# Optimization experiments

Hardware: AMD Instinct MI355X
Metric: run time of the kernel (lower is better)

The kernel has to match this reference:

```python
import jax, jax.numpy as jnp
import numpy as np

F_DIM = 64      # self.n_atom_basis inside blocks (= n_atom_basis // 2)
N_LAYERS = 2
N_RBF = 20
CUTOFF = 5.0
EPS = 1e-8
N_ATOMS = 15000
N_PAIRS = 300000


def setup_inputs() -> dict:
    key = jax.random.key(0)
    ks = jax.random.split(key, 20)
    def w(k, shape, fan_in):
        return (jax.random.normal(k, shape, dtype=jnp.float32) / np.float32(np.sqrt(fan_in)))
    F, L, R = F_DIM, N_LAYERS, N_RBF
    return {
        "Z": jax.random.randint(ks[0], (N_ATOMS,), 0, 100),
        "Rij": jax.random.normal(ks[1], (N_PAIRS, 3), dtype=jnp.float32),
        "idx_i": jax.random.randint(ks[2], (N_PAIRS,), 0, N_ATOMS),
        "idx_j": jax.random.randint(ks[3], (N_PAIRS,), 0, N_ATOMS),
        "n_atoms": N_ATOMS,
        "embed": w(ks[4], (100, F), 1.0),
        "filter_W": w(ks[5], (R, L * 3 * F), R),
        "filter_b": jnp.zeros((L * 3 * F,), jnp.float32),
        "ctx_W1": w(ks[6], (L, F, F), F),
        "ctx_b1": jnp.zeros((L, F), jnp.float32),
        "ctx_W2": w(ks[7], (L, F, 3 * F), F),
        "ctx_b2": jnp.zeros((L, 3 * F), jnp.float32),
        "comp_W1": w(ks[8], (L, 2 * F, 32), 2 * F),
        "comp_b1": jnp.zeros((L, 32), jnp.float32),
        "comp_W2": w(ks[9], (L, 32, F), 32),
        "comp_b2": jnp.zeros((L, F), jnp.float32),
        "rec_W1": w(ks[10], (L, F, 32), F),
        "rec_b1": jnp.zeros((L, 32), jnp.float32),
        "rec_W2": w(ks[11], (L, 32, F * F), 32),
        "rec_b2": jnp.zeros((L, F * F), jnp.float32),
        "mix_W1": w(ks[12], (L, 2 * F, F), 2 * F),
        "mix_b1": jnp.zeros((L, F), jnp.float32),
        "mix_W2": w(ks[13], (L, F, 3 * F), F),
        "mix_b2": jnp.zeros((L, 3 * F), jnp.float32),
        "mu_mix_W": w(ks[14], (L, F, 2 * F), F),
    }


def _compress(v, W1, b1, W2, b2):
    # v: [..., 3, C]  (xyz axis = -2). Per-channel vector norm -> MLP -> softmax weights.
    s = jnp.sqrt(jnp.sum(v * v, axis=-2) + EPS)                      # [..., C]
    wts = jax.nn.softmax(jnp.maximum(s @ W1 + b1, 0.0) @ W2 + b2, axis=-1)  # [..., Fc]
    # einsum('bvc,bl->blc') == weights (outer) sum_over_channels(v)
    return jnp.sum(v, axis=-1, keepdims=True) * wts[..., None, :]    # [..., 3, Fc]


def _interaction(q, mu, Wij, dir_ij, idx_i, idx_j, n_atoms,
                 cW1, cb1, cW2, cb2, pW1, pb1, pW2, pb2, rW1, rb1, rW2, rb2):
    F = q.shape[-1]
    x = jax.nn.silu(q @ cW1 + cb1) @ cW2 + cb2                       # [n,1,3F]
    xe = x[idx_j] * Wij                                               # [p,1,3F] gather + filter mult
    dq, dmuR, dmumu = jnp.split(xe, 3, axis=-1)
    dq = jax.ops.segment_sum(dq, idx_i, num_segments=n_atoms)        # [n,1,F]
    cvj = _compress(mu[idx_j], pW1, pb1, pW2, pb2)                    # [p,3,F]
    dmu = dmuR * dir_ij[:, :, None] + dmumu * cvj                     # [p,3,F]
    dmu = jax.ops.segment_sum(dmu, idx_i, num_segments=n_atoms)       # [n,3,F]
    cvi = _compress(mu, pW1, pb1, pW2, pb2)                           # [n,3,F]
    q = q + dq
    mu = dmu + cvi                                                    # [n,3,F]
    # reconstruction layer -> rank-2 tensors per channel
    cv = jnp.swapaxes(mu, 1, 2)                                       # [n,F,3]
    s = jnp.sqrt(jnp.sum(mu * mu, axis=1) + EPS)                      # [n,F]
    sw = (jnp.maximum(s @ rW1 + rb1, 0.0) @ rW2 + rb2).reshape(-1, F, F)
    dtm = jnp.einsum('nrc,nci,ncj->nrij', sw, cv, cv)                 # [n,F,3,3]
    return q, mu, dtm


def _mixing(q, mu, dtm, W1, b1, W2, b2, Wm):
    mu_mix = mu @ Wm                                                  # [n,3,2F]
    mu_V, mu_W = jnp.split(mu_mix, 2, axis=-1)
    mu_Vn = jnp.sqrt(jnp.sum(mu_V * mu_V, axis=-2, keepdims=True) + EPS)  # [n,1,F]
    x = jax.nn.silu(jnp.concatenate([q, mu_Vn], axis=-1) @ W1 + b1) @ W2 + b2
    dq_i, dmu_i, dqmu_i = jnp.split(x, 3, axis=-1)
    dmu_i = dmu_i * mu_W
    dqmu_i = dqmu_i * jnp.sum(mu_V * mu_W, axis=1, keepdims=True)
    q = q + dq_i + dqmu_i                                             # [n,1,F]
    tv = jnp.einsum('nfij,njf->nif', dtm, mu)                         # [n,3,F]
    mu = jnp.concatenate([mu + dmu_i, tv], axis=-1)                   # [n,3,2F]
    return q, mu


def _forward(Z, Rij, idx_i, idx_j, n_atoms, embed, filter_W, filter_b,
             ctx_W1, ctx_b1, ctx_W2, ctx_b2, comp_W1, comp_b1, comp_W2, comp_b2,
             rec_W1, rec_b1, rec_W2, rec_b2, mix_W1, mix_b1, mix_W2, mix_b2, mu_mix_W):
    F = embed.shape[1]
    d = jnp.linalg.norm(Rij, axis=1, keepdims=True)                   # [p,1]
    dir_ij = Rij / d                                                  # [p,3]
    offsets = jnp.linspace(0.0, CUTOFF, N_RBF).astype(jnp.float32)
    width = offsets[1] - offsets[0]
    phi = jnp.exp(-0.5 * ((d[..., None] - offsets) / width) ** 2)     # [p,1,R]
    fcut = 0.5 * (jnp.cos(jnp.pi * d / CUTOFF) + 1.0) * (d < CUTOFF)  # [p,1]
    filters = (phi @ filter_W + filter_b) * fcut[..., None]           # [p,1,L*3F]
    q = embed[Z][:, None, :]                                          # [n,1,F]
    mu = jnp.zeros((q.shape[0], 3, 2 * F), q.dtype)                   # [n,3,2F]
    for l in range(ctx_W1.shape[0]):
        Wij = filters[..., l * 3 * F:(l + 1) * 3 * F]
        q, mu, dtm = _interaction(q, mu, Wij, dir_ij, idx_i, idx_j, n_atoms,
                                  ctx_W1[l], ctx_b1[l], ctx_W2[l], ctx_b2[l],
                                  comp_W1[l], comp_b1[l], comp_W2[l], comp_b2[l],
                                  rec_W1[l], rec_b1[l], rec_W2[l], rec_b2[l])
        q, mu = _mixing(q, mu, dtm, mix_W1[l], mix_b1[l], mix_W2[l], mix_b2[l], mu_mix_W[l])
    return q[:, 0, :], mu  # scalar_representation [n,F], vector_representation [n,3,2F]


def reference(Z, Rij, idx_i, idx_j, n_atoms, embed, filter_W, filter_b,
              ctx_W1, ctx_b1, ctx_W2, ctx_b2, comp_W1, comp_b1, comp_W2, comp_b2,
              rec_W1, rec_b1, rec_W2, rec_b2, mix_W1, mix_b1, mix_W2, mix_b2, mu_mix_W):
    return _forward(Z, Rij, idx_i, idx_j, n_atoms, embed, filter_W, filter_b,
                    ctx_W1, ctx_b1, ctx_W2, ctx_b2, comp_W1, comp_b1, comp_W2, comp_b2,
                    rec_W1, rec_b1, rec_W2, rec_b2, mix_W1, mix_b1, mix_W2, mix_b2, mu_mix_W)
```

## Files before the change

### kernel.cpp

```cpp
#include <hip/hip_runtime.h>
#include <math.h>

#define FD 64
#define NRBF 20
#define CUT 5.0f
#define EPSV 1e-8f
#define PI_F 3.14159265358979f

typedef _Float16 h2v __attribute__((ext_vector_type(2)));

__device__ __forceinline__ float wredsum(float v){
#pragma unroll
  for (int m = 32; m >= 1; m >>= 1) v += __shfl_xor(v, m, 64);
  return v;
}
__device__ __forceinline__ float wredmax(float v){
#pragma unroll
  for (int m = 32; m >= 1; m >>= 1) v = fmaxf(v, __shfl_xor(v, m, 64));
  return v;
}
__device__ __forceinline__ float silu_f(float x){ return x * (1.0f / (1.0f + __expf(-x))); }
__device__ __forceinline__ h2v as_h2(unsigned u){
  union { unsigned u; h2v h; } x; x.u = u; return x.h;
}
__device__ __forceinline__ unsigned pack_bf16(float a, float b){
  unsigned ua = __float_as_uint(a), ub = __float_as_uint(b);
  ua = (ua + 0x7fffu + ((ua >> 16) & 1u)) >> 16;
  ub = (ub + 0x7fffu + ((ub >> 16) & 1u)) >> 16;
  return ua | (ub << 16);
}
__device__ __forceinline__ unsigned pack_f16(float a, float b){
  return __builtin_bit_cast(unsigned, __builtin_amdgcn_cvt_pkrtz(a, b));
}
#define BF_LO(u) __uint_as_float((u) << 16)
#define BF_HI(u) __uint_as_float((u) & 0xffff0000u)

__global__ __launch_bounds__(256) void k_count(const int* __restrict__ idx_i,
                                               int* __restrict__ cnt, int P)
{
  int p = blockIdx.x * blockDim.x + threadIdx.x;
  if (p < P) atomicAdd(&cnt[idx_i[p]], 1);
}

__global__ __launch_bounds__(1024) void k_scan(const int* __restrict__ cnt,
                                               int* __restrict__ start,
                                               int* __restrict__ cursor, int N)
{
  __shared__ int part[1024];
  int t = threadIdx.x;
  int chunk = (N + 1023) / 1024;
  int lo = t * chunk, hi = lo + chunk; if (hi > N) hi = N;
  int s = 0;
  for (int i = lo; i < hi; ++i) s += cnt[i];
  part[t] = s;
  __syncthreads();
  for (int off = 1; off < 1024; off <<= 1){
    int v = 0;
    if (t >= off) v = part[t - off];
    __syncthreads();
    if (t >= off) part[t] += v;
    __syncthreads();
  }
  int run = (t == 0) ? 0 : part[t-1];
  for (int i = lo; i < hi; ++i){ start[i] = run; cursor[i] = run; run += cnt[i]; }
  if (t == 1023) start[N] = run;
}

__global__ __launch_bounds__(256) void k_scatter(const int* __restrict__ idx_i,
                                                 int* __restrict__ cursor,
                                                 int* __restrict__ elist, int P)
{
  int p = blockIdx.x * blockDim.x + threadIdx.x;
  if (p < P){
    int pos = atomicAdd(&cursor[idx_i[p]], 1);
    elist[pos] = p;
  }
}

__global__ __launch_bounds__(256) void k_edgeprep(const float* __restrict__ Rij,
                                                  const int* __restrict__ elist,
                                                  const int* __restrict__ idx_j,
                                                  float* __restrict__ eP,
                                                  int* __restrict__ eJ, int P)
{
  int e = blockIdx.x * blockDim.x + threadIdx.x;
  if (e >= P) return;
  int p = elist[e];
  eJ[e] = idx_j[p];
  float rx = Rij[3*p+0], ry = Rij[3*p+1], rz = Rij[3*p+2];
  float d = sqrtf(rx*rx + ry*ry + rz*rz);
  float inv = 1.0f / d;
  float fc = (d < CUT) ? 0.5f * (__cosf(PI_F * d / CUT) + 1.0f) : 0.0f;
  float* pr = eP + (size_t)e * 16;
  pr[0] = rx*inv; pr[1] = ry*inv; pr[2] = rz*inv; pr[3] = fc;
  const float width = CUT / (float)(NRBF - 1);
  float ph[NRBF];
#pragma unroll
  for (int r = 0; r < NRBF; ++r){
    float t = (d - width * (float)r) / width;
    ph[r] = __expf(-0.5f * t * t) * fc;
  }
  unsigned* pu = (unsigned*)(pr + 4);
#pragma unroll
  for (int r = 0; r < 10; ++r) pu[r] = pack_f16(ph[2*r], ph[2*r+1]);
  pr[14] = 0.f; pr[15] = 0.f;
}

__global__ __launch_bounds__(256) void k_transpose_w(const float* __restrict__ rW2,
                                                     const float* __restrict__ rb2,
                                                     unsigned short* __restrict__ rW2S,
                                                     float* __restrict__ rb2T)
{
  int t = blockIdx.x * blockDim.x + threadIdx.x;
  if (t < 2*64*64*32){
    int km = t & 7;
    int f  = (t >> 3) & 63;
    int kq = (t >> 9) & 3;
    int c  = (t >> 11) & 63;
    int l  = t >> 17;
    int k  = kq*8 + km;
    float v = rW2[((size_t)(l*32 + k))*4096 + f*64 + c];
    _Float16 hv = (_Float16)v;
    unsigned short us;
    __builtin_memcpy(&us, &hv, 2);
    rW2S[t] = us;
  }
  if (t < 2*64*64){
    int f = t & 63, c = (t >> 6) & 63, l = t >> 12;
    rb2T[t] = rb2[(size_t)l*4096 + f*64 + c];
  }
}

__global__ __launch_bounds__(256) void k_init_q(const int* __restrict__ Z,
                                                const float* __restrict__ embed,
                                                float* __restrict__ q, int Ntot)
{
  int t = blockIdx.x * blockDim.x + threadIdx.x;
  if (t >= Ntot * FD) return;
  int n = t >> 6, f = t & 63;
  q[t] = embed[Z[n]*FD + f];
}

__global__ __launch_bounds__(256) void k_atom_pre(
    const float* __restrict__ q, const float* __restrict__ mu,
    const float* __restrict__ cW1, const float* __restrict__ cb1,
    const float* __restrict__ cW2, const float* __restrict__ cb2,
    const float* __restrict__ pW1, const float* __restrict__ pb1,
    const float* __restrict__ pW2, const float* __restrict__ pb2,
    unsigned* __restrict__ XCVh, float* __restrict__ CVf, int Ntot)
{
  __shared__ float wbuf[12288];
  __shared__ float qs[16][64];
  __shared__ float sbuf[16][128];
  __shared__ float h1s[16][64];
  __shared__ float hcs[16][32];
  int t = threadIdx.x;
  int w = t >> 6, f = t & 63;
  int base = blockIdx.x * 16;
  const int aw = w * 4;
  float4* wt4 = (float4*)wbuf;

  float m0a[4], m1a[4], m2a[4], m0b[4], m1b[4], m2b[4];
#pragma unroll
  for (int s = 0; s < 4; ++s){
    int a = aw + s;
    int n = base + a; if (n >= Ntot) n = Ntot - 1;
    qs[a][f] = q[(size_t)n*64 + f];
    const float* mun = mu + (size_t)n * 384;
    m0a[s] = mun[0*128 + f];      m1a[s] = mun[1*128 + f];      m2a[s] = mun[2*128 + f];
    m0b[s] = mun[0*128 + 64 + f]; m1b[s] = mun[1*128 + 64 + f]; m2b[s] = mun[2*128 + 64 + f];
    sbuf[a][f]      = sqrtf(m0a[s]*m0a[s] + m1a[s]*m1a[s] + m2a[s]*m2a[s] + EPSV);
    sbuf[a][64 + f] = sqrtf(m0b[s]*m0b[s] + m1b[s]*m1b[s] + m2b[s]*m2b[s] + EPSV);
  }
#pragma unroll
  for (int i = 0; i < 4; ++i) wt4[t + i*256] = ((const float4*)cW1)[t + i*256];
  __syncthreads();

  float hacc[4];
#pragma unroll
  for (int s = 0; s < 4; ++s) hacc[s] = cb1[f];
  for (int k = 0; k < 64; ++k){
    float wv = wbuf[k*64 + f];
#pragma unroll
    for (int s = 0; s < 4; ++s) hacc[s] = fmaf(qs[aw + s][k], wv, hacc[s]);
  }
#pragma unroll
  for (int s = 0; s < 4; ++s) h1s[aw + s][f] = silu_f(hacc[s]);

  __syncthreads();
#pragma unroll
  for (int i = 0; i < 12; ++i) wt4[t + i*256] = ((const float4*)cW2)[t + i*256];
  __syncthreads();

  float x0[4], x1[4], x2[4];
#pragma unroll
  for (int s = 0; s < 4; ++s){ x0[s] = cb2[f]; x1[s] = cb2[64+f]; x2[s] = cb2[128+f]; }
  for (int k = 0; k < 64; ++k){
    float u0 = wbuf[k*192 + f];
    float u1 = wbuf[k*192 + 64 + f];
    float u2 = wbuf[k*192 + 128 + f];
#pragma unroll
    for (int s = 0; s < 4; ++s){
      float h = h1s[aw + s][k];
      x0[s] = fmaf(h, u0, x0[s]); x1[s] = fmaf(h, u1, x1[s]); x2[s] = fmaf(h, u2, x2[s]);
    }
  }
#pragma unroll
  for (int s = 0; s < 4; ++s){
    int n = base + aw + s;
    if (n < Ntot) XCVh[(size_t)n*192 + f] = pack_bf16(x0[s], x1[s]);
  }

  __syncthreads();
#pragma unroll
  for (int i = 0; i < 4; ++i) wt4[t + i*256] = ((const float4*)pW1)[t + i*256];
#pragma unroll
  for (int i = 0; i < 2; ++i) wt4[1024 + t + i*256] = ((const float4*)pW2)[t + i*256];
  __syncthreads();

  int ki = f & 31;
#pragma unroll
  for (int p = 0; p < 2; ++p){
    int a_h = aw + p*2 + (f >> 5);
    float ah = pb1[ki];
#pragma unroll 4
    for (int c = 0; c < 128; ++c) ah = fmaf(sbuf[a_h][c], wbuf[c*32 + ki], ah);
    hcs[a_h][ki] = fmaxf(ah, 0.0f);
  }

  float logit[4];
#pragma unroll
  for (int s = 0; s < 4; ++s) logit[s] = pb2[f];
  for (int k = 0; k < 32; ++k){
    float wv = wbuf[4096 + k*64 + f];
#pragma unroll
    for (int s = 0; s < 4; ++s) logit[s] = fmaf(hcs[aw + s][k], wv, logit[s]);
  }
#pragma unroll
  for (int s = 0; s < 4; ++s){
    float mx = wredmax(logit[s]);
    float e  = __expf(logit[s] - mx);
    float se = wredsum(e);
    float wt = e / se;
    float v0 = wredsum(m0a[s] + m0b[s]);
    float v1 = wredsum(m1a[s] + m1b[s]);
    float v2 = wredsum(m2a[s] + m2b[s]);
    int n = base + aw + s;
    if (n < Ntot){
      float cv0 = v0 * wt, cv1 = v1 * wt, cv2 = v2 * wt;
      XCVh[(size_t)n*192 + 64 + f]  = pack_bf16(x2[s], cv0);
      XCVh[(size_t)n*192 + 128 + f] = pack_bf16(cv1, cv2);
      float* cvn = CVf + (size_t)n*192;
      cvn[f] = cv0; cvn[64+f] = cv1; cvn[128+f] = cv2;
    }
  }
}

__global__ __launch_bounds__(256) void k_gather(
    const float* __restrict__ eP, const int* __restrict__ eJ,
    const int* __restrict__ start,
    const float* __restrict__ fW, const float* __restrict__ fb,
    const unsigned* __restrict__ XCVh,
    float* __restrict__ dq, float* __restrict__ dmu, int l, int Ntot)
{
  int w = threadIdx.x >> 6;
  int f = threadIdx.x & 63;
  int i = blockIdx.x * 4 + w;
  if (i >= Ntot) return;
  const int col = l * 192;

  unsigned fwp0[10], fwp1[10], fwp2[10];
#pragma unroll
  for (int r = 0; r < 10; ++r){
    const float* fa = fW + (2*r)*384 + col;
    const float* fbp = fW + (2*r+1)*384 + col;
    fwp0[r] = pack_f16(fa[f],       fbp[f]);
    fwp1[r] = pack_f16(fa[64 + f],  fbp[64 + f]);
    fwp2[r] = pack_f16(fa[128 + f], fbp[128 + f]);
  }
  float fb0 = fb[col + f], fb1 = fb[col + 64 + f], fb2 = fb[col + 128 + f];

  float dqa = 0.f, dm0 = 0.f, dm1 = 0.f, dm2 = 0.f;
  int e0 = start[i], e1 = start[i+1];
  int e = e0;
  for (; e + 4 <= e1; e += 4){
    int jj[4];
    float4 d4[4];
    uint4  p0[4], p1[4], p2[4];
    unsigned xv0[4], xv1[4], xv2[4];
#pragma unroll
    for (int u = 0; u < 4; ++u) jj[u] = eJ[e + u];
#pragma unroll
    for (int u = 0; u < 4; ++u){
      const float4* pr = (const float4*)(eP + (size_t)(e + u) * 16);
      const uint4*  pui = (const uint4*)pr;
      d4[u] = pr[0]; p0[u] = pui[1]; p1[u] = pui[2]; p2[u] = pui[3];
    }
#pragma unroll
    for (int u = 0; u < 4; ++u){
      const unsigned* xj = XCVh + (size_t)jj[u] * 192;
      xv0[u] = xj[f]; xv1[u] = xj[64 + f]; xv2[u] = xj[128 + f];
    }
#pragma unroll
    for (int u = 0; u < 4; ++u){
      unsigned ph[10] = {p0[u].x,p0[u].y,p0[u].z,p0[u].w,
                         p1[u].x,p1[u].y,p1[u].z,p1[u].w,
                         p2[u].x,p2[u].y};
      float fc = d4[u].w;
      float w0 = fb0 * fc, w1 = fb1 * fc, w2 = fb2 * fc;
#pragma unroll
      for (int r = 0; r < 10; ++r){
        w0 = __builtin_amdgcn_fdot2(as_h2(ph[r]), as_h2(fwp0[r]), w0, false);
        w1 = __builtin_amdgcn_fdot2(as_h2(ph[r]), as_h2(fwp1[r]), w1, false);
        w2 = __builtin_amdgcn_fdot2(as_h2(ph[r]), as_h2(fwp2[r]), w2, false);
      }
      dqa = fmaf(BF_LO(xv0[u]), w0, dqa);
      float dmR = BF_HI(xv0[u]) * w1, dmm = BF_LO(xv1[u]) * w2;
      dm0 = fmaf(dmR, d4[u].x, fmaf(dmm, BF_HI(xv1[u]), dm0));
      dm1 = fmaf(dmR, d4[u].y, fmaf(dmm, BF_LO(xv2[u]), dm1));
      dm2 = fmaf(dmR, d4[u].z, fmaf(dmm, BF_HI(xv2[u]), dm2));
    }
  }
  for (; e < e1; ++e){
    int j = eJ[e];
    const float4* pr = (const float4*)(eP + (size_t)e * 16);
    const uint4*  pu = (const uint4*)pr;
    float4 A0 = pr[0];
    uint4  Ap0 = pu[1], Ap1 = pu[2], Ap2 = pu[3];
    const unsigned* xj = XCVh + (size_t)j * 192;
    unsigned u0=xj[f], u1=xj[64+f], u2=xj[128+f];
    unsigned ph[10] = {Ap0.x,Ap0.y,Ap0.z,Ap0.w, Ap1.x,Ap1.y,Ap1.z,Ap1.w, Ap2.x,Ap2.y};
    float w0 = fb0 * A0.w, w1 = fb1 * A0.w, w2 = fb2 * A0.w;
#pragma unroll
    for (int r = 0; r < 10; ++r){
      w0 = __builtin_amdgcn_fdot2(as_h2(ph[r]), as_h2(fwp0[r]), w0, false);
      w1 = __builtin_amdgcn_fdot2(as_h2(ph[r]), as_h2(fwp1[r]), w1, false);
      w2 = __builtin_amdgcn_fdot2(as_h2(ph[r]), as_h2(fwp2[r]), w2, false);
    }
    dqa = fmaf(BF_LO(u0), w0, dqa);
    float dmR = BF_HI(u0) * w1, dmm = BF_LO(u1) * w2;
    dm0 = fmaf(dmR, A0.x, fmaf(dmm, BF_HI(u1), dm0));
    dm1 = fmaf(dmR, A0.y, fmaf(dmm, BF_LO(u2), dm1));
    dm2 = fmaf(dmR, A0.z, fmaf(dmm, BF_HI(u2), dm2));
  }
  dq[(size_t)i*64 + f] = dqa;
  float* dmn = dmu + (size_t)i*192;
  dmn[f] = dm0; dmn[64 + f] = dm1; dmn[128 + f] = dm2;
}

__global__ __launch_bounds__(512) void k_tv(
    const float* __restrict__ dmuA, const float* __restrict__ CVf,
    const float* __restrict__ rW1, const float* __restrict__ rb1,
    const unsigned short* __restrict__ rW2S, const float* __restrict__ rb2Tl,
    float* __restrict__ MUI, float* __restrict__ TV, int Ntot)
{
  __shared__ float mus[16][3][64];
  __shared__ float svs[16][64];
  __shared__ float4 wt4[2048];
  __shared__ float rbt[8][64];
  int t = threadIdx.x;
  int w = t >> 6, f = t & 63;
  int base = blockIdx.x * 16;

#pragma unroll
  for (int s = 0; s < 2; ++s){
    int a = w*2 + s;
    int n = base + a; bool ok = (n < Ntot); if (!ok) n = Ntot - 1;
    const float* dmn = dmuA + (size_t)n*192;
    const float* cvn = CVf  + (size_t)n*192;
    float m0 = dmn[f]       + cvn[f];
    float m1 = dmn[64 + f]  + cvn[64 + f];
    float m2 = dmn[128 + f] + cvn[128 + f];
    mus[a][0][f] = m0; mus[a][1][f] = m1; mus[a][2][f] = m2;
    svs[a][f] = sqrtf(m0*m0 + m1*m1 + m2*m2 + EPSV);
    if (ok){
      float* mo = MUI + (size_t)n*192;
      mo[f] = m0; mo[64+f] = m1; mo[128+f] = m2;
    }
  }
  __syncthreads();

  int ki = f & 31;
  int a_h = w*2 + (f >> 5);
  float ah = rb1[ki];
#pragma unroll
  for (int c = 0; c < 64; ++c) ah = fmaf(svs[a_h][c], rW1[c*32 + ki], ah);
  ah = fmaxf(ah, 0.0f);
  unsigned hpk0[16], hpk1[16];
#pragma unroll
  for (int k = 0; k < 16; ++k){
    float a0 = __shfl(ah, 2*k, 64),      b0 = __shfl(ah, 2*k + 1, 64);
    float a1 = __shfl(ah, 32 + 2*k, 64), b1 = __shfl(ah, 32 + 2*k + 1, 64);
    hpk0[k] = pack_f16(a0, b0);
    hpk1[k] = pack_f16(a1, b1);
  }

  const int a0i = w*2, a1i = a0i + 1;
  float mf00 = mus[a0i][0][f], mf01 = mus[a0i][1][f], mf02 = mus[a0i][2][f];
  float mf10 = mus[a1i][0][f], mf11 = mus[a1i][1][f], mf12 = mus[a1i][2][f];
  float tv00=0,tv01=0,tv02=0, tv10=0,tv11=0,tv12=0;
  const uint4* wtu = reinterpret_cast<const uint4*>(wt4);

  for (int ct = 0; ct < 8; ++ct){
    __syncthreads();
    const float4* src = (const float4*)rW2S + (size_t)ct*2048;
#pragma unroll
    for (int i = 0; i < 4; ++i) wt4[t + i*512] = src[t + i*512];
    if (t < 128) ((float4*)rbt)[t] = ((const float4*)(rb2Tl + ct*512))[t];
    __syncthreads();

#pragma unroll
    for (int cc = 0; cc < 8; ++cc){
      int c = ct*8 + cc;
      float u00 = mus[a0i][0][c], u01 = mus[a0i][1][c], u02 = mus[a0i][2][c];
      float u10 = mus[a1i][0][c], u11 = mus[a1i][1][c], u12 = mus[a1i][2][c];
      float g0 = u00*mf00 + u01*mf01 + u02*mf02;
      float g1 = u10*mf10 + u11*mf11 + u12*mf12;
      float acc0 = rbt[cc][f];
      float acc1 = acc0;
#pragma unroll
      for (int kq = 0; kq < 4; ++kq){
        uint4 u = wtu[(cc*4 + kq)*64 + f];
        int k0 = kq*4;
        acc0 = __builtin_amdgcn_fdot2(as_h2(u.x), as_h2(hpk0[k0+0]), acc0, false);
        acc0 = __builtin_amdgcn_fdot2(as_h2(u.y), as_h2(hpk0[k0+1]), acc0, false);
        acc0 = __builtin_amdgcn_fdot2(as_h2(u.z), as_h2(hpk0[k0+2]), acc0, false);
        acc0 = __builtin_amdgcn_fdot2(as_h2(u.w), as_h2(hpk0[k0+3]), acc0, false);
        acc1 = __builtin_amdgcn_fdot2(as_h2(u.x), as_h2(hpk1[k0+0]), acc1, false);
        acc1 = __builtin_amdgcn_fdot2(as_h2(u.y), as_h2(hpk1[k0+1]), acc1, false);
        acc1 = __builtin_amdgcn_fdot2(as_h2(u.z), as_h2(hpk1[k0+2]), acc1, false);
        acc1 = __builtin_amdgcn_fdot2(as_h2(u.w), as_h2(hpk1[k0+3]), acc1, false);
      }
      float mm0 = acc0 * g0, mm1 = acc1 * g1;
      tv00 = fmaf(u00, mm0, tv00); tv01 = fmaf(u01, mm0, tv01); tv02 = fmaf(u02, mm0, tv02);
      tv10 = fmaf(u10, mm1, tv10); tv11 = fmaf(u11, mm1, tv11); tv12 = fmaf(u12, mm1, tv12);
    }
  }

  int n0 = base + a0i, n1 = base + a1i;
  if (n0 < Ntot){
    float* tvp = TV + (size_t)n0*192;
    tvp[f] = tv00; tvp[64+f] = tv01; tvp[128+f] = tv02;
  }
  if (n1 < Ntot){
    float* tvp = TV + (size_t)n1*192;
    tvp[f] = tv10; tvp[64+f] = tv11; tvp[128+f] = tv12;
  }
}

__global__ __launch_bounds__(256) void k_mix2(
    float* __restrict__ q, float* __restrict__ mu,
    const float* __restrict__ dq, const float* __restrict__ MUI, const float* __restrict__ TV,
    const float* __restrict__ mW1, const float* __restrict__ mb1,
    const float* __restrict__ mW2, const float* __restrict__ mb2,
    const float* __restrict__ Wm, int Ntot)
{
  __shared__ float wbuf[12288];
  __shared__ float mua[16][3][64];
  __shared__ float ava[16][128];
  __shared__ float h2a[16][64];
  int t = threadIdx.x;
  int w = t >> 6, f = t & 63;
  int base = blockIdx.x * 16;
  const int aw = w * 4;
  float4* wt4 = (float4*)wbuf;

  float qv[4], m0[4], m1[4], m2[4];
#pragma unroll
  for (int s = 0; s < 4; ++s){
    int a = aw + s;
    int n = base + a; if (n >= Ntot) n = Ntot - 1;
    qv[s] = q[(size_t)n*64 + f] + dq[(size_t)n*64 + f];
    const float* mi = MUI + (size_t)n*192;
    m0[s] = mi[f]; m1[s] = mi[64 + f]; m2[s] = mi[128 + f];
    mua[a][0][f] = m0[s]; mua[a][1][f] = m1[s]; mua[a][2][f] = m2[s];
  }

#pragma unroll
  for (int i = 0; i < 8; ++i) wt4[t + i*256] = ((const float4*)Wm)[t + i*256];
  __syncthreads();

  float V0[4]={0,0,0,0}, V1[4]={0,0,0,0}, V2[4]={0,0,0,0};
  float W0[4]={0,0,0,0}, W1[4]={0,0,0,0}, W2[4]={0,0,0,0};
  for (int k = 0; k < 64; ++k){
    float wv = wbuf[k*128 + f];
    float ww = wbuf[k*128 + 64 + f];
#pragma unroll
    for (int s = 0; s < 4; ++s){
      int a = aw + s;
      float b0 = mua[a][0][k], b1 = mua[a][1][k], b2 = mua[a][2][k];
      V0[s] = fmaf(b0, wv, V0[s]); V1[s] = fmaf(b1, wv, V1[s]); V2[s] = fmaf(b2, wv, V2[s]);
      W0[s] = fmaf(b0, ww, W0[s]); W1[s] = fmaf(b1, ww, W1[s]); W2[s] = fmaf(b2, ww, W2[s]);
    }
  }
  float dot[4];
#pragma unroll
  for (int s = 0; s < 4; ++s){
    int a = aw + s;
    ava[a][f] = qv[s];
    ava[a][64 + f] = sqrtf(V0[s]*V0[s] + V1[s]*V1[s] + V2[s]*V2[s] + EPSV);
    dot[s] = V0[s]*W0[s] + V1[s]*W1[s] + V2[s]*W2[s];
  }

  __syncthreads();
#pragma unroll
  for (int i = 0; i < 8; ++i) wt4[t + i*256] = ((const float4*)mW1)[t + i*256];
  __syncthreads();

  float acc[4];
#pragma unroll
  for (int s = 0; s < 4; ++s) acc[s] = mb1[f];
  for (int k = 0; k < 128; ++k){
    float wv = wbuf[k*64 + f];
#pragma unroll
    for (int s = 0; s < 4; ++s) acc[s] = fmaf(ava[aw + s][k], wv, acc[s]);
  }
#pragma unroll
  for (int s = 0; s < 4; ++s) h2a[aw + s][f] = silu_f(acc[s]);

  __syncthreads();
#pragma unroll
  for (int i = 0; i < 12; ++i) wt4[t + i*256] = ((const float4*)mW2)[t + i*256];
  __syncthreads();

  float y0[4], y1[4], y2[4];
#pragma unroll
  for (int s = 0; s < 4; ++s){ y0[s] = mb2[f]; y1[s] = mb2[64+f]; y2[s] = mb2[128+f]; }
  for (int k = 0; k < 64; ++k){
    float u0 = wbuf[k*192 + f];
    float u1 = wbuf[k*192 + 64 + f];
    float u2 = wbuf[k*192 + 128 + f];
#pragma unroll
    for (int s = 0; s < 4; ++s){
      float h = h2a[aw + s][k];
      y0[s] = fmaf(h, u0, y0[s]); y1[s] = fmaf(h, u1, y1[s]); y2[s] = fmaf(h, u2, y2[s]);
    }
  }

#pragma unroll
  for (int s = 0; s < 4; ++s){
    int n = base + aw + s;
    if (n < Ntot){
      q[(size_t)n*64 + f] = qv[s] + y0[s] + y2[s]*dot[s];
      const float* tvp = TV + (size_t)n*192;
      float* mun = mu + (size_t)n*384;
      mun[0*128 + f] = fmaf(y1[s], W0[s], m0[s]); mun[0*128 + 64 + f] = tvp[f];
      mun[1*128 + f] = fmaf(y1[s], W1[s], m1[s]); mun[1*128 + 64 + f] = tvp[64+f];
      mun[2*128 + f] = fmaf(y1[s], W2[s], m2[s]); mun[2*128 + 64 + f] = tvp[128+f];
    }
  }
}

extern "C" void kernel_launch(void* const* d_in, const int* in_sizes, int n_in,
                              void* d_out, int out_size, void* d_ws, size_t ws_size,
                              hipStream_t stream)
{
  const int*   Z      = (const int*)  d_in[0];
  const float* Rij    = (const float*)d_in[1];
  const int*   idx_i  = (const int*)  d_in[2];
  const int*   idx_j  = (const int*)  d_in[3];
  const float* embed  = (const float*)d_in[5];
  const float* fW     = (const float*)d_in[6];
  const float* fb     = (const float*)d_in[7];
  const float* ctxW1  = (const float*)d_in[8];
  const float* ctxb1  = (const float*)d_in[9];
  const float* ctxW2  = (const float*)d_in[10];
  const float* ctxb2  = (const float*)d_in[11];
  const float* compW1 = (const float*)d_in[12];
  const float* compb1 = (const float*)d_in[13];
  const float* compW2 = (const float*)d_in[14];
  const float* compb2 = (const float*)d_in[15];
  const float* recW1  = (const float*)d_in[16];
  const float* recb1  = (const float*)d_in[17];
  const float* recW2  = (const float*)d_in[18];
  const float* recb2  = (const float*)d_in[19];
  const float* mixW1  = (const float*)d_in[20];
  const float* mixb1  = (const float*)d_in[21];
  const float* mixW2  = (const float*)d_in[22];
  const float* mixb2  = (const float*)d_in[23];
  const float* muMixW = (const float*)d_in[24];

  const int N = in_sizes[0];
  const int P = in_sizes[1] / 3;

  float* ws    = (float*)d_ws;
  float* eP    = ws;
  float* q     = eP    + (size_t)P*16;
  float* mu    = q     + (size_t)N*64;
  float* XCVhf = mu    + (size_t)N*384;
  float* CVf   = XCVhf + (size_t)N*192;
  float* dq    = CVf   + (size_t)N*192;
  float* dmu   = dq    + (size_t)N*64;
  float* rW2Sf = dmu   + (size_t)N*192;
  float* rb2T  = rW2Sf + (size_t)131072;
  float* TV    = rb2T  + (size_t)8192;
  float* MUI   = TV    + (size_t)N*192;
  int*   cnt    = (int*)(MUI + (size_t)N*192);
  int*   startA = cnt    + N;
  int*   cursor = startA + (N + 1);
  int*   elist  = cursor + N;
  int*   eJ     = elist  + P;
  unsigned*       XCVh = (unsigned*)XCVhf;
  unsigned short* rW2S = (unsigned short*)rW2Sf;

  hipMemsetAsync(mu, 0, (size_t)N*384*sizeof(float), stream);
  hipMemsetAsync(cnt, 0, (size_t)N*sizeof(int), stream);
  k_init_q<<<(N*FD + 255)/256, 256, 0, stream>>>(Z, embed, q, N);
  k_transpose_w<<<(2*64*64*32 + 255)/256, 256, 0, stream>>>(recW2, recb2, rW2S, rb2T);

  k_count<<<(P + 255)/256, 256, 0, stream>>>(idx_i, cnt, P);
  k_scan<<<1, 1024, 0, stream>>>(cnt, startA, cursor, N);
  k_scatter<<<(P + 255)/256, 256, 0, stream>>>(idx_i, cursor, elist, P);
  k_edgeprep<<<(P + 255)/256, 256, 0, stream>>>(Rij, elist, idx_j, eP, eJ, P);

  const int ablk4  = (N + 3) / 4;
  const int ablk16 = (N + 15) / 16;
  for (int l = 0; l < 2; ++l){
    k_atom_pre<<<ablk16, 256, 0, stream>>>(q, mu,
        ctxW1 + (size_t)l*64*64,  ctxb1 + (size_t)l*64,
        ctxW2 + (size_t)l*64*192, ctxb2 + (size_t)l*192,
        compW1 + (size_t)l*128*32, compb1 + (size_t)l*32,
        compW2 + (size_t)l*32*64,  compb2 + (size_t)l*64,
        XCVh, CVf, N);
    k_gather<<<ablk4, 256, 0, stream>>>(eP, eJ, startA, fW, fb, XCVh,
        dq, dmu, l, N);
    k_tv<<<ablk16, 512, 0, stream>>>(dmu, CVf,
        recW1 + (size_t)l*64*32, recb1 + (size_t)l*32,
        rW2S + (size_t)l*131072, rb2T + (size_t)l*4096,
        MUI, TV, N);
    k_mix2<<<ablk16, 256, 0, stream>>>(q, mu, dq, MUI, TV,
        mixW1 + (size_t)l*128*64, mixb1 + (size_t)l*64,
        mixW2 + (size_t)l*64*192, mixb2 + (size_t)l*192,
        muMixW + (size_t)l*64*128, N);
  }

  hipMemcpyAsync(d_out, q, (size_t)N*64*sizeof(float), hipMemcpyDeviceToDevice, stream);
  hipMemcpyAsync((float*)d_out + (size_t)N*64, mu, (size_t)N*384*sizeof(float),
                 hipMemcpyDeviceToDevice, stream);
}
```

Baseline: 530.5 us.

## Fuse tensor-vector and mixing kernels into one post-interaction kernel

```diff
diff --git a/kernel.cpp b/kernel.cpp
--- a/kernel.cpp
+++ b/kernel.cpp
@@ -348,43 +348,52 @@
   dmn[f] = dm0; dmn[64 + f] = dm1; dmn[128 + f] = dm2;
 }
 
-__global__ __launch_bounds__(512) void k_tv(
-    const float* __restrict__ dmuA, const float* __restrict__ CVf,
+__global__ __launch_bounds__(512) void k_post(
+    float* __restrict__ q, float* __restrict__ mu,
+    const float* __restrict__ dq, const float* __restrict__ dmuA,
+    const float* __restrict__ CVf,
     const float* __restrict__ rW1, const float* __restrict__ rb1,
     const unsigned short* __restrict__ rW2S, const float* __restrict__ rb2Tl,
-    float* __restrict__ MUI, float* __restrict__ TV, int Ntot)
+    const float* __restrict__ mW1, const float* __restrict__ mb1,
+    const float* __restrict__ mW2, const float* __restrict__ mb2,
+    const float* __restrict__ Wm, int Ntot)
 {
   __shared__ float mus[16][3][64];
-  __shared__ float svs[16][64];
-  __shared__ float4 wt4[2048];
-  __shared__ float rbt[8][64];
+  __shared__ float svr[2048];
+  __shared__ float wbuf[8192];
   int t = threadIdx.x;
   int w = t >> 6, f = t & 63;
   int base = blockIdx.x * 16;
-
+  float4* wt4 = (float4*)wbuf;
+  float* svs = svr;
+  float* rbt = svr + 1024;
+  float* ava = svr;
+  float* h2a = (float*)mus;
+
+  const int a0i = w*2, a1i = a0i + 1;
+
+  float qv0, qv1;
 #pragma unroll
   for (int s = 0; s < 2; ++s){
-    int a = w*2 + s;
-    int n = base + a; bool ok = (n < Ntot); if (!ok) n = Ntot - 1;
+    int a = a0i + s;
+    int n = base + a; if (n >= Ntot) n = Ntot - 1;
     const float* dmn = dmuA + (size_t)n*192;
     const float* cvn = CVf  + (size_t)n*192;
     float m0 = dmn[f]       + cvn[f];
     float m1 = dmn[64 + f]  + cvn[64 + f];
     float m2 = dmn[128 + f] + cvn[128 + f];
     mus[a][0][f] = m0; mus[a][1][f] = m1; mus[a][2][f] = m2;
-    svs[a][f] = sqrtf(m0*m0 + m1*m1 + m2*m2 + EPSV);
-    if (ok){
-      float* mo = MUI + (size_t)n*192;
-      mo[f] = m0; mo[64+f] = m1; mo[128+f] = m2;
-    }
+    svs[a*64 + f] = sqrtf(m0*m0 + m1*m1 + m2*m2 + EPSV);
+    float qn = q[(size_t)n*64 + f] + dq[(size_t)n*64 + f];
+    if (s == 0) qv0 = qn; else qv1 = qn;
   }
   __syncthreads();
 
   int ki = f & 31;
-  int a_h = w*2 + (f >> 5);
+  int a_h = a0i + (f >> 5);
   float ah = rb1[ki];
 #pragma unroll
-  for (int c = 0; c < 64; ++c) ah = fmaf(svs[a_h][c], rW1[c*32 + ki], ah);
+  for (int c = 0; c < 64; ++c) ah = fmaf(svs[a_h*64 + c], rW1[c*32 + ki], ah);
   ah = fmaxf(ah, 0.0f);
   unsigned hpk0[16], hpk1[16];
 #pragma unroll
@@ -395,7 +404,6 @@
     hpk1[k] = pack_f16(a1, b1);
   }
 
-  const int a0i = w*2, a1i = a0i + 1;
   float mf00 = mus[a0i][0][f], mf01 = mus[a0i][1][f], mf02 = mus[a0i][2][f];
   float mf10 = mus[a1i][0][f], mf11 = mus[a1i][1][f], mf12 = mus[a1i][2][f];
   float tv00=0,tv01=0,tv02=0, tv10=0,tv11=0,tv12=0;
@@ -416,138 +424,111 @@
       float u10 = mus[a1i][0][c], u11 = mus[a1i][1][c], u12 = mus[a1i][2][c];
       float g0 = u00*mf00 + u01*mf01 + u02*mf02;
       float g1 = u10*mf10 + u11*mf11 + u12*mf12;
-      float acc0 = rbt[cc][f];
-      float acc1 = acc0;
-#pragma unroll
-      for (int kq = 0; kq < 4; ++kq){
-        uint4 u = wtu[(cc*4 + kq)*64 + f];
-        int k0 = kq*4;
-        acc0 = __builtin_amdgcn_fdot2(as_h2(u.x), as_h2(hpk0[k0+0]), acc0, false);
-        acc0 = __builtin_amdgcn_fdot2(as_h2(u.y), as_h2(hpk0[k0+1]), acc0, false);
-        acc0 = __builtin_amdgcn_fdot2(as_h2(u.z), as_h2(hpk0[k0+2]), acc0, false);
-        acc0 = __builtin_amdgcn_fdot2(as_h2(u.w), as_h2(hpk0[k0+3]), acc0, false);
-        acc1 = __builtin_amdgcn_fdot2(as_h2(u.x), as_h2(hpk1[k0+0]), acc1, false);
-        acc1 = __builtin_amdgcn_fdot2(as_h2(u.y), as_h2(hpk1[k0+1]), acc1, false);
-        acc1 = __builtin_amdgcn_fdot2(as_h2(u.z), as_h2(hpk1[k0+2]), acc1, false);
-        acc1 = __builtin_amdgcn_fdot2(as_h2(u.w), as_h2(hpk1[k0+3]), acc1, false);
+      float a0A = rbt[cc*64 + f], a0B = 0.f;
+      float a1A = a0A,            a1B = 0.f;
+      uint4 uA = wtu[(cc*4 + 0)*64 + f];
+      uint4 uB = wtu[(cc*4 + 2)*64 + f];
+#pragma unroll
+      for (int x = 0; x < 4; ++x){
+        unsigned wA = (&uA.x)[x], wB = (&uB.x)[x];
+        a0A = __builtin_amdgcn_fdot2(as_h2(wA), as_h2(hpk0[x]),     a0A, false);
+        a0B = __builtin_amdgcn_fdot2(as_h2(wB), as_h2(hpk0[8 + x]), a0B, false);
+        a1A = __builtin_amdgcn_fdot2(as_h2(wA), as_h2(hpk1[x]),     a1A, false);
+        a1B = __builtin_amdgcn_fdot2(as_h2(wB), as_h2(hpk1[8 + x]), a1B, false);
       }
-      float mm0 = acc0 * g0, mm1 = acc1 * g1;
+      uA = wtu[(cc*4 + 1)*64 + f];
+      uB = wtu[(cc*4 + 3)*64 + f];
+#pragma unroll
+      for (int x = 0; x < 4; ++x){
+        unsigned wA = (&uA.x)[x], wB = (&uB.x)[x];
+        a0A = __builtin_amdgcn_fdot2(as_h2(wA), as_h2(hpk0[4 + x]),  a0A, false);
+        a0B = __builtin_amdgcn_fdot2(as_h2(wB), as_h2(hpk0[12 + x]), a0B, false);
+        a1A = __builtin_amdgcn_fdot2(as_h2(wA), as_h2(hpk1[4 + x]),  a1A, false);
+        a1B = __builtin_amdgcn_fdot2(as_h2(wB), as_h2(hpk1[12 + x]), a1B, false);
+      }
+      float mm0 = (a0A + a0B) * g0, mm1 = (a1A + a1B) * g1;
       tv00 = fmaf(u00, mm0, tv00); tv01 = fmaf(u01, mm0, tv01); tv02 = fmaf(u02, mm0, tv02);
       tv10 = fmaf(u10, mm1, tv10); tv11 = fmaf(u11, mm1, tv11); tv12 = fmaf(u12, mm1, tv12);
     }
   }
 
-  int n0 = base + a0i, n1 = base + a1i;
-  if (n0 < Ntot){
-    float* tvp = TV + (size_t)n0*192;
-    tvp[f] = tv00; tvp[64+f] = tv01; tvp[128+f] = tv02;
-  }
-  if (n1 < Ntot){
-    float* tvp = TV + (size_t)n1*192;
-    tvp[f] = tv10; tvp[64+f] = tv11; tvp[128+f] = tv12;
-  }
-}
-
-__global__ __launch_bounds__(256) void k_mix2(
-    float* __restrict__ q, float* __restrict__ mu,
-    const float* __restrict__ dq, const float* __restrict__ MUI, const float* __restrict__ TV,
-    const float* __restrict__ mW1, const float* __restrict__ mb1,
-    const float* __restrict__ mW2, const float* __restrict__ mb2,
-    const float* __restrict__ Wm, int Ntot)
-{
-  __shared__ float wbuf[12288];
-  __shared__ float mua[16][3][64];
-  __shared__ float ava[16][128];
-  __shared__ float h2a[16][64];
-  int t = threadIdx.x;
-  int w = t >> 6, f = t & 63;
-  int base = blockIdx.x * 16;
-  const int aw = w * 4;
-  float4* wt4 = (float4*)wbuf;
-
-  float qv[4], m0[4], m1[4], m2[4];
-#pragma unroll
-  for (int s = 0; s < 4; ++s){
-    int a = aw + s;
-    int n = base + a; if (n >= Ntot) n = Ntot - 1;
-    qv[s] = q[(size_t)n*64 + f] + dq[(size_t)n*64 + f];
-    const float* mi = MUI + (size_t)n*192;
-    m0[s] = mi[f]; m1[s] = mi[64 + f]; m2[s] = mi[128 + f];
-    mua[a][0][f] = m0[s]; mua[a][1][f] = m1[s]; mua[a][2][f] = m2[s];
-  }
-
-#pragma unroll
-  for (int i = 0; i < 8; ++i) wt4[t + i*256] = ((const float4*)Wm)[t + i*256];
-  __syncthreads();
-
-  float V0[4]={0,0,0,0}, V1[4]={0,0,0,0}, V2[4]={0,0,0,0};
-  float W0[4]={0,0,0,0}, W1[4]={0,0,0,0}, W2[4]={0,0,0,0};
+  __syncthreads();
+#pragma unroll
+  for (int i = 0; i < 4; ++i) wt4[t + i*512] = ((const float4*)Wm)[t + i*512];
+  __syncthreads();
+
+  float V00=0,V01=0,V02=0, W00=0,W01=0,W02=0;
+  float V10=0,V11=0,V12=0, W10=0,W11=0,W12=0;
   for (int k = 0; k < 64; ++k){
     float wv = wbuf[k*128 + f];
     float ww = wbuf[k*128 + 64 + f];
-#pragma unroll
-    for (int s = 0; s < 4; ++s){
-      int a = aw + s;
-      float b0 = mua[a][0][k], b1 = mua[a][1][k], b2 = mua[a][2][k];
-      V0[s] = fmaf(b0, wv, V0[s]); V1[s] = fmaf(b1, wv, V1[s]); V2[s] = fmaf(b2, wv, V2[s]);
-      W0[s] = fmaf(b0, ww, W0[s]); W1[s] = fmaf(b1, ww, W1[s]); W2[s] = fmaf(b2, ww, W2[s]);
-    }
-  }
-  float dot[4];
-#pragma unroll
-  for (int s = 0; s < 4; ++s){
-    int a = aw + s;
-    ava[a][f] = qv[s];
-    ava[a][64 + f] = sqrtf(V0[s]*V0[s] + V1[s]*V1[s] + V2[s]*V2[s] + EPSV);
-    dot[s] = V0[s]*W0[s] + V1[s]*W1[s] + V2[s]*W2[s];
-  }
-
-  __syncthreads();
-#pragma unroll
-  for (int i = 0; i < 8; ++i) wt4[t + i*256] = ((const float4*)mW1)[t + i*256];
-  __syncthreads();
-
-  float acc[4];
-#pragma unroll
-  for (int s = 0; s < 4; ++s) acc[s] = mb1[f];
+    float b00 = mus[a0i][0][k], b01 = mus[a0i][1][k], b02 = mus[a0i][2][k];
+    float b10 = mus[a1i][0][k], b11 = mus[a1i][1][k], b12 = mus[a1i][2][k];
+    V00 = fmaf(b00, wv, V00); V01 = fmaf(b01, wv, V01); V02 = fmaf(b02, wv, V02);
+    W00 = fmaf(b00, ww, W00); W01 = fmaf(b01, ww, W01); W02 = fmaf(b02, ww, W02);
+    V10 = fmaf(b10, wv, V10); V11 = fmaf(b11, wv, V11); V12 = fmaf(b12, wv, V12);
+    W10 = fmaf(b10, ww, W10); W11 = fmaf(b11, ww, W11); W12 = fmaf(b12, ww, W12);
+  }
+  float dot0 = V00*W00 + V01*W01 + V02*W02;
+  float dot1 = V10*W10 + V11*W11 + V12*W12;
+  __syncthreads();
+  ava[a0i*128 + f] = qv0; ava[a0i*128 + 64 + f] = sqrtf(V00*V00 + V01*V01 + V02*V02 + EPSV);
+  ava[a1i*128 + f] = qv1; ava[a1i*128 + 64 + f] = sqrtf(V10*V10 + V11*V11 + V12*V12 + EPSV);
+#pragma unroll
+  for (int i = 0; i < 4; ++i) wt4[t + i*512] = ((const float4*)mW1)[t + i*512];
+  __syncthreads();
+
+  float acc0 = mb1[f], acc1 = acc0;
   for (int k = 0; k < 128; ++k){
     float wv = wbuf[k*64 + f];
-#pragma unroll
-    for (int s = 0; s < 4; ++s) acc[s] = fmaf(ava[aw + s][k], wv, acc[s]);
-  }
-#pragma unroll
-  for (int s = 0; s < 4; ++s) h2a[aw + s][f] = silu_f(acc[s]);
-
-  __syncthreads();
-#pragma unroll
-  for (int i = 0; i < 12; ++i) wt4[t + i*256] = ((const float4*)mW2)[t + i*256];
-  __syncthreads();
-
-  float y0[4], y1[4], y2[4];
-#pragma unroll
-  for (int s = 0; s < 4; ++s){ y0[s] = mb2[f]; y1[s] = mb2[64+f]; y2[s] = mb2[128+f]; }
-  for (int k = 0; k < 64; ++k){
+    acc0 = fmaf(ava[a0i*128 + k], wv, acc0);
+    acc1 = fmaf(ava[a1i*128 + k], wv, acc1);
+  }
+  __syncthreads();
+  h2a[a0i*64 + f] = silu_f(acc0);
+  h2a[a1i*64 + f] = silu_f(acc1);
+
+  float y00 = mb2[f], y01 = mb2[64+f], y02 = mb2[128+f];
+  float y10 = y00, y11 = y01, y12 = y02;
+  __syncthreads();
+#pragma unroll
+  for (int i = 0; i < 3; ++i) wt4[t + i*512] = ((const float4*)mW2)[t + i*512];
+  __syncthreads();
+  for (int k = 0; k < 32; ++k){
     float u0 = wbuf[k*192 + f];
     float u1 = wbuf[k*192 + 64 + f];
     float u2 = wbuf[k*192 + 128 + f];
-#pragma unroll
-    for (int s = 0; s < 4; ++s){
-      float h = h2a[aw + s][k];
-      y0[s] = fmaf(h, u0, y0[s]); y1[s] = fmaf(h, u1, y1[s]); y2[s] = fmaf(h, u2, y2[s]);
-    }
-  }
-
-#pragma unroll
-  for (int s = 0; s < 4; ++s){
-    int n = base + aw + s;
-    if (n < Ntot){
-      q[(size_t)n*64 + f] = qv[s] + y0[s] + y2[s]*dot[s];
-      const float* tvp = TV + (size_t)n*192;
-      float* mun = mu + (size_t)n*384;
-      mun[0*128 + f] = fmaf(y1[s], W0[s], m0[s]); mun[0*128 + 64 + f] = tvp[f];
-      mun[1*128 + f] = fmaf(y1[s], W1[s], m1[s]); mun[1*128 + 64 + f] = tvp[64+f];
-      mun[2*128 + f] = fmaf(y1[s], W2[s], m2[s]); mun[2*128 + 64 + f] = tvp[128+f];
-    }
+    float h0 = h2a[a0i*64 + k], h1 = h2a[a1i*64 + k];
+    y00 = fmaf(h0, u0, y00); y01 = fmaf(h0, u1, y01); y02 = fmaf(h0, u2, y02);
+    y10 = fmaf(h1, u0, y10); y11 = fmaf(h1, u1, y11); y12 = fmaf(h1, u2, y12);
+  }
+  __syncthreads();
+#pragma unroll
+  for (int i = 0; i < 3; ++i) wt4[t + i*512] = ((const float4*)(mW2 + 6144))[t + i*512];
+  __syncthreads();
+  for (int k = 0; k < 32; ++k){
+    float u0 = wbuf[k*192 + f];
+    float u1 = wbuf[k*192 + 64 + f];
+    float u2 = wbuf[k*192 + 128 + f];
+    float h0 = h2a[a0i*64 + 32 + k], h1 = h2a[a1i*64 + 32 + k];
+    y00 = fmaf(h0, u0, y00); y01 = fmaf(h0, u1, y01); y02 = fmaf(h0, u2, y02);
+    y10 = fmaf(h1, u0, y10); y11 = fmaf(h1, u1, y11); y12 = fmaf(h1, u2, y12);
+  }
+
+  int n0 = base + a0i, n1 = base + a1i;
+  if (n0 < Ntot){
+    q[(size_t)n0*64 + f] = qv0 + y00 + y02*dot0;
+    float* mun = mu + (size_t)n0*384;
+    mun[0*128 + f] = fmaf(y01, W00, mf00); mun[0*128 + 64 + f] = tv00;
+    mun[1*128 + f] = fmaf(y01, W01, mf01); mun[1*128 + 64 + f] = tv01;
+    mun[2*128 + f] = fmaf(y01, W02, mf02); mun[2*128 + 64 + f] = tv02;
+  }
+  if (n1 < Ntot){
+    q[(size_t)n1*64 + f] = qv1 + y10 + y12*dot1;
+    float* mun = mu + (size_t)n1*384;
+    mun[0*128 + f] = fmaf(y11, W10, mf10); mun[0*128 + 64 + f] = tv10;
+    mun[1*128 + f] = fmaf(y11, W11, mf11); mun[1*128 + 64 + f] = tv11;
+    mun[2*128 + f] = fmaf(y11, W12, mf12); mun[2*128 + 64 + f] = tv12;
   }
 }
 
@@ -593,9 +574,7 @@
   float* dmu   = dq    + (size_t)N*64;
   float* rW2Sf = dmu   + (size_t)N*192;
   float* rb2T  = rW2Sf + (size_t)131072;
-  float* TV    = rb2T  + (size_t)8192;
-  float* MUI   = TV    + (size_t)N*192;
-  int*   cnt    = (int*)(MUI + (size_t)N*192);
+  int*   cnt    = (int*)(rb2T + (size_t)8192);
   int*   startA = cnt    + N;
   int*   cursor = startA + (N + 1);
   int*   elist  = cursor + N;
@@ -624,11 +603,9 @@
         XCVh, CVf, N);
     k_gather<<<ablk4, 256, 0, stream>>>(eP, eJ, startA, fW, fb, XCVh,
         dq, dmu, l, N);
-    k_tv<<<ablk16, 512, 0, stream>>>(dmu, CVf,
+    k_post<<<ablk16, 512, 0, stream>>>(q, mu, dq, dmu, CVf,
         recW1 + (size_t)l*64*32, recb1 + (size_t)l*32,
         rW2S + (size_t)l*131072, rb2T + (size_t)l*4096,
-        MUI, TV, N);
-    k_mix2<<<ablk16, 256, 0, stream>>>(q, mu, dq, MUI, TV,
         mixW1 + (size_t)l*128*64, mixb1 + (size_t)l*64,
         mixW2 + (size_t)l*64*192, mixb2 + (size_t)l*192,
         muMixW + (size_t)l*64*128, N);
```

New measurement: 941.9 us. +77.6%, slower.
